# Kernel tuning notes

Measured on AMD Instinct MI355X. Metric: run time of the kernel, lower is better.

## Reference

```python
import jax, jax.numpy as jnp
import numpy as np

B, N, F, D, M, R, K, TOPR = 32, 1024, 10, 64, 4, 8, 20, 2
TAU = 1.0
BN_EPS = 1e-5


def setup_inputs() -> dict:
    key = jax.random.key(0)
    ks = jax.random.split(key, 20)
    s = 0.1
    p = {}
    p['data'] = jax.random.normal(ks[0], (B, N, F), jnp.float32)
    u = jnp.clip(jax.random.uniform(ks[1], (B, M), jnp.float32), 1e-6, 1.0 - 1e-6)
    p['gumbel_noise'] = -jnp.log(-jnp.log(u))
    p['W_cond'] = jax.random.normal(ks[2], (F, D), jnp.float32) * s
    p['b_cond'] = jnp.zeros((D,), jnp.float32)
    p['W_ap'] = jax.random.normal(ks[3], (D, D), jnp.float32) * s
    p['b_ap'] = jnp.zeros((D,), jnp.float32)
    p['W_av'] = jax.random.normal(ks[4], (D, 1), jnp.float32) * s
    p['W_r'] = jax.random.normal(ks[5], (D, M), jnp.float32) * s
    p['b_r'] = jnp.zeros((M,), jnp.float32)
    p['e_base'] = jax.random.normal(ks[6], (N, D), jnp.float32) * s
    p['lr_u'] = jax.random.normal(ks[7], (M, N, R), jnp.float32) * s
    p['lr_v'] = jax.random.normal(ks[8], (M, R, D), jnp.float32) * s
    p['W_gnn'] = jax.random.normal(ks[9], (F, D), jnp.float32) * s
    p['att_i'] = jax.random.normal(ks[10], (D,), jnp.float32) * s
    p['att_j'] = jax.random.normal(ks[11], (D,), jnp.float32) * s
    p['att_em_i'] = jax.random.normal(ks[12], (D,), jnp.float32) * s
    p['att_em_j'] = jax.random.normal(ks[13], (D,), jnp.float32) * s
    p['b_gnn'] = jnp.zeros((D,), jnp.float32)
    p['bn1_gamma'] = jnp.ones((D,), jnp.float32)
    p['bn1_beta'] = jnp.zeros((D,), jnp.float32)
    p['node_embed_table'] = jax.random.normal(ks[14], (N, D), jnp.float32) * s
    p['bn_out_gamma'] = jnp.ones((D,), jnp.float32)
    p['bn_out_beta'] = jnp.zeros((D,), jnp.float32)
    p['W_out'] = jax.random.normal(ks[15], (D, 1), jnp.float32) * s
    p['b_out'] = jnp.zeros((1,), jnp.float32)
    return p


def _nan(x):
    return jnp.nan_to_num(x, nan=0.0, posinf=1e4, neginf=-1e4)


def _bn(x, gamma, beta, axes):
    # BatchNorm1d in training mode: biased batch stats over `axes`.
    mu = x.mean(axes, keepdims=True)
    var = x.var(axes, keepdims=True)
    return (x - mu) * jax.lax.rsqrt(var + BN_EPS) * gamma + beta


def reference(data, gumbel_noise, W_cond, b_cond, W_ap, b_ap, W_av, W_r, b_r,
              e_base, lr_u, lr_v, W_gnn, att_i, att_j, att_em_i, att_em_j,
              b_gnn, bn1_gamma, bn1_beta, node_embed_table,
              bn_out_gamma, bn_out_beta, W_out, b_out):
    x_det = jax.lax.stop_gradient(data)                      # data.clone().detach()
    # --- condition attention pooling ---
    h_it = data @ W_cond + b_cond                            # [B,N,D]
    ah = jax.nn.leaky_relu(h_it @ W_ap + b_ap, 0.2)
    e_it = _nan((ah @ W_av)[..., 0])                         # [B,N]
    beta = jax.nn.softmax(e_it, axis=1)
    h_sys = jnp.sum(beta[..., None] * h_it, axis=1)          # [B,D]
    # --- gumbel top-k routing with straight-through ---
    pi_soft = jax.nn.softmax((h_sys @ W_r + b_r + gumbel_noise) / TAU, axis=-1)
    topv, topi = jax.lax.top_k(pi_soft, TOPR)
    pi_hard = jnp.sum(jax.nn.one_hot(topi, M, dtype=pi_soft.dtype) * topv[..., None], axis=1)
    pi_hard = pi_hard / jnp.maximum(pi_hard.sum(-1, keepdims=True), 1e-12)
    pi_t = jax.lax.stop_gradient(pi_hard - pi_soft) + pi_soft
    # --- low-rank expert prototypes -> mixed node embeddings ---
    proto = e_base[None] + jnp.einsum('mnr,mrd->mnd', lr_u, lr_v)    # [M,N,D]
    mixed = _nan(jnp.einsum('bm,mnd->bnd', pi_t, proto))             # [B,N,D]
    # --- dynamic top-k graph construction ---
    scores = _nan(jnp.einsum('bid,bjd->bij', mixed, mixed))          # [B,N,N]
    topk_vals, topk_idx = jax.lax.top_k(scores, K)                   # src nodes per dst: [B,N,K]
    topk_w = jax.nn.softmax(topk_vals, axis=-1)                      # edge weights
    # --- GAT-style layer with embedding-augmented keys, self loops re-added ---
    x_lin = x_det @ W_gnn                                            # [B,N,D]
    s_i = x_lin @ att_i + mixed @ att_em_i                           # [B,N]
    s_j = x_lin @ att_j + mixed @ att_em_j
    sj_nb = jnp.take_along_axis(s_j, topk_idx.reshape(B, N * K), axis=1).reshape(B, N, K)
    self_mask = topk_idx == jnp.arange(N)[None, :, None]             # remove_self_loops on topk edges
    alpha_nb = jnp.where(self_mask, -jnp.inf, jax.nn.leaky_relu(s_i[:, :, None] + sj_nb, 0.2))
    alpha_self = jax.nn.leaky_relu(s_i + s_j, 0.2)
    att = jax.nn.softmax(jnp.concatenate([alpha_nb, alpha_self[..., None]], axis=-1), axis=-1)
    w_nb = att[..., :K] * topk_w                                     # edge_weight modulation
    w_self = att[..., K]
    x_src = jnp.take_along_axis(x_lin, topk_idx.reshape(B, N * K)[..., None], axis=1).reshape(B, N, K, D)
    gnn = jnp.einsum('bnk,bnkd->bnd', w_nb, x_src) + w_self[..., None] * x_lin + b_gnn
    gnn = jax.nn.relu(_bn(gnn.reshape(B * N, D), bn1_gamma, bn1_beta, 0).reshape(B, N, D))
    # --- output head ---
    out = gnn * node_embed_table[None]                               # [B,N,D]
    out = jax.nn.relu(_bn(out, bn_out_gamma, bn_out_beta, (0, 1)))   # dropout = identity (eval)
    out = (out @ W_out + b_out).reshape(-1, N)                       # [B,N]
    return out, h_sys, pi_soft
```

## Files before the change

### kernel.cpp

```cpp
#include <hip/hip_runtime.h>
#include <math.h>

#define BB 32
#define NN 1024
#define FF 10
#define DD 64
#define MM 4
#define RR 8
#define KK 20
#define BNROWS (BB*NN)

#define OFF_HIT   0ull
#define OFF_XLIN  2097152ull
#define OFF_EIT   4194304ull
#define OFF_PIT   4227072ull
#define OFF_MIXED 4227200ull
#define OFF_SI    6324352ull
#define OFF_SJ    6357120ull
#define OFF_TKV   6389888ull
#define OFF_TKI   7045248ull
#define OFF_GNN   7700608ull
#define OFF_OUTP  9797760ull
#define OFF_STAT  11894912ull
#define OFF_SC    (OFF_STAT + 2560ull)

__device__ __forceinline__ float wave_sum(float v) {
    #pragma unroll
    for (int off = 32; off; off >>= 1) v += __shfl_xor(v, off);
    return v;
}
__device__ __forceinline__ float wave_max(float v) {
    #pragma unroll
    for (int off = 32; off; off >>= 1) v = fmaxf(v, __shfl_xor(v, off));
    return v;
}

__device__ __forceinline__ unsigned int dpp_wave_max_u32(unsigned int x) {
    unsigned int t;
    t = (unsigned)__builtin_amdgcn_update_dpp(0, (int)x, 0x111, 0xF, 0xF, true);
    x = x > t ? x : t;
    t = (unsigned)__builtin_amdgcn_update_dpp(0, (int)x, 0x112, 0xF, 0xF, true);
    x = x > t ? x : t;
    t = (unsigned)__builtin_amdgcn_update_dpp(0, (int)x, 0x114, 0xF, 0xF, true);
    x = x > t ? x : t;
    t = (unsigned)__builtin_amdgcn_update_dpp(0, (int)x, 0x118, 0xF, 0xF, true);
    x = x > t ? x : t;
    t = (unsigned)__builtin_amdgcn_update_dpp(0, (int)x, 0x142, 0xF, 0xF, true);
    x = x > t ? x : t;
    t = (unsigned)__builtin_amdgcn_update_dpp(0, (int)x, 0x143, 0xF, 0xF, true);
    x = x > t ? x : t;
    return (unsigned)__builtin_amdgcn_readlane((int)x, 63);
}

__global__ __launch_bounds__(256) void k_rows(
    const float* __restrict__ data, const float* __restrict__ W_cond,
    const float* __restrict__ b_cond, const float* __restrict__ W_ap,
    const float* __restrict__ b_ap, const float* __restrict__ W_av,
    const float* __restrict__ W_gnn,
    float* __restrict__ h_it, float* __restrict__ x_lin, float* __restrict__ e_it,
    float* __restrict__ stats)
{
    if (blockIdx.x < 10) {
        int idx = blockIdx.x * 256 + threadIdx.x;
        if (idx < 2336) stats[idx] = 0.f;
    }
    int w = threadIdx.x >> 6, lane = threadIdx.x & 63;
    int r = blockIdx.x * 4 + w;
    const float* dr = data + r * FF;
    float df[FF];
    #pragma unroll
    for (int f = 0; f < FF; f++) df[f] = dr[f];
    float h = b_cond[lane], x = 0.f;
    #pragma unroll
    for (int f = 0; f < FF; f++) {
        h = fmaf(df[f], W_cond[f * DD + lane], h);
        x = fmaf(df[f], W_gnn[f * DD + lane], x);
    }
    h_it[r * DD + lane] = h;
    x_lin[r * DD + lane] = x;
    float acc = b_ap[lane];
    #pragma unroll
    for (int e2 = 0; e2 < DD; e2++)
        acc = fmaf(__shfl(h, e2), W_ap[e2 * DD + lane], acc);
    float lr = acc > 0.f ? acc : 0.2f * acc;
    float ep = wave_sum(lr * W_av[lane]);
    if (lane == 0) e_it[r] = ep;
}

__global__ __launch_bounds__(256) void k_pool2(
    const float* __restrict__ e_it, const float* __restrict__ h_it,
    float* __restrict__ num, float* __restrict__ den)
{
    int w = threadIdx.x >> 6, lane = threadIdx.x & 63;
    int b = blockIdx.x >> 3, ch = blockIdx.x & 7;
    int base = b * NN + ch * 128 + w * 32;
    float acc = 0.f, dn = 0.f;
    #pragma unroll 4
    for (int i = 0; i < 32; i++) {
        float e = e_it[base + i];
        float wgt = expf(e);
        acc = fmaf(wgt, h_it[(size_t)(base + i) * DD + lane], acc);
        dn += wgt;
    }
    __shared__ float pa[4][DD];
    __shared__ float pd[4];
    pa[w][lane] = acc;
    if (lane == 0) pd[w] = dn;
    __syncthreads();
    if (w == 0) {
        float s = pa[0][lane] + pa[1][lane] + pa[2][lane] + pa[3][lane];
        atomicAdd(&num[b * DD + lane], s);
        if (lane == 0) atomicAdd(&den[b], pd[0] + pd[1] + pd[2] + pd[3]);
    }
}

__global__ void k_route(const float* __restrict__ num, const float* __restrict__ den,
                        const float* __restrict__ W_r, const float* __restrict__ b_r,
                        const float* __restrict__ gumbel,
                        float* __restrict__ h_sys, float* __restrict__ pi_soft,
                        float* __restrict__ pi_t)
{
    int tid = threadIdx.x;
    for (int i = tid; i < BB * DD; i += 256)
        h_sys[i] = num[i] / den[i >> 6];
    if (tid >= BB) return;
    int b = tid;
    float inv = 1.0f / den[b];
    float lg[MM];
    #pragma unroll
    for (int m = 0; m < MM; m++) lg[m] = b_r[m] + gumbel[b * MM + m];
    for (int d = 0; d < DD; d++) {
        float hv = num[b * DD + d] * inv;
        #pragma unroll
        for (int m = 0; m < MM; m++) lg[m] = fmaf(hv, W_r[d * MM + m], lg[m]);
    }
    float mx = fmaxf(fmaxf(lg[0], lg[1]), fmaxf(lg[2], lg[3]));
    float s = 0.f, p[MM];
    #pragma unroll
    for (int m = 0; m < MM; m++) { p[m] = expf(lg[m] - mx); s += p[m]; }
    #pragma unroll
    for (int m = 0; m < MM; m++) { p[m] /= s; pi_soft[b * MM + m] = p[m]; }
    int i1 = 0; float v1 = p[0];
    #pragma unroll
    for (int m = 1; m < MM; m++) if (p[m] > v1) { v1 = p[m]; i1 = m; }
    int i2 = -1; float v2 = -1.f;
    #pragma unroll
    for (int m = 0; m < MM; m++) if (m != i1 && p[m] > v2) { v2 = p[m]; i2 = m; }
    float norm = fmaxf(v1 + v2, 1e-12f);
    #pragma unroll
    for (int m = 0; m < MM; m++)
        pi_t[b * MM + m] = (m == i1 ? v1 : (m == i2 ? v2 : 0.f)) / norm;
}

__global__ __launch_bounds__(256) void k_mixed(
    const float* __restrict__ e_base, const float* __restrict__ lr_u,
    const float* __restrict__ lr_v, const float* __restrict__ pi_t,
    const float* __restrict__ x_lin,
    const float* __restrict__ att_i, const float* __restrict__ att_j,
    const float* __restrict__ att_em_i, const float* __restrict__ att_em_j,
    float* __restrict__ mixed, float* __restrict__ s_i, float* __restrict__ s_j)
{
    int w = threadIdx.x >> 6, lane = threadIdx.x & 63;
    int r = blockIdx.x * 4 + w;
    int b = r >> 10, n = r & 1023;
    float LR[MM];
    #pragma unroll
    for (int m = 0; m < MM; m++) {
        float a = 0.f;
        #pragma unroll
        for (int rr = 0; rr < RR; rr++)
            a = fmaf(lr_u[(m * NN + n) * RR + rr], lr_v[(m * RR + rr) * DD + lane], a);
        LR[m] = a;
    }
    float eb = e_base[n * DD + lane];
    float mx = 0.f;
    #pragma unroll
    for (int m = 0; m < MM; m++) mx = fmaf(pi_t[b * MM + m], eb + LR[m], mx);
    mixed[(size_t)r * DD + lane] = mx;
    float x = x_lin[(size_t)r * DD + lane];
    float r1 = wave_sum(x * att_i[lane] + mx * att_em_i[lane]);
    float r2 = wave_sum(x * att_j[lane] + mx * att_em_j[lane]);
    if (lane == 0) { s_i[r] = r1; s_j[r] = r2; }
}

__global__ __launch_bounds__(256) void k_score(
    const float* __restrict__ mixed_chunk, float* __restrict__ sc)
{
    __shared__ float As[32 * 132];
    __shared__ float Bs[32 * 132];
    int t = threadIdx.x;
    int bb = blockIdx.x >> 6;
    int rr = blockIdx.x & 63;
    int it = rr >> 3, jt = rr & 7;
    int i0 = it * 128, j0 = jt * 128;
    const float* mb = mixed_chunk + (size_t)bb * NN * DD;

    int tx = t & 15, ty = t >> 4;
    float acc[8][8];
    #pragma unroll
    for (int a = 0; a < 8; a++)
        #pragma unroll
        for (int bj = 0; bj < 8; bj++) acc[a][bj] = 0.f;

    for (int hh = 0; hh < 2; hh++) {
        if (hh) __syncthreads();
        #pragma unroll
        for (int c = 0; c < 4; c++) {
            int id = t + c * 256;
            int row = (id & 15) | ((id >> 7) << 4);
            int q = (id >> 4) & 7;
            const float4 va = *(const float4*)(mb + (size_t)(i0 + row) * DD + hh * 32 + q * 4);
            As[(q * 4 + 0) * 132 + row] = va.x;
            As[(q * 4 + 1) * 132 + row] = va.y;
            As[(q * 4 + 2) * 132 + row] = va.z;
            As[(q * 4 + 3) * 132 + row] = va.w;
            const float4 vb = *(const float4*)(mb + (size_t)(j0 + row) * DD + hh * 32 + q * 4);
            Bs[(q * 4 + 0) * 132 + row] = vb.x;
            Bs[(q * 4 + 1) * 132 + row] = vb.y;
            Bs[(q * 4 + 2) * 132 + row] = vb.z;
            Bs[(q * 4 + 3) * 132 + row] = vb.w;
        }
        __syncthreads();
        #pragma unroll 4
        for (int d = 0; d < 32; d++) {
            float4 a0 = *(const float4*)&As[d * 132 + ty * 8];
            float4 a1 = *(const float4*)&As[d * 132 + ty * 8 + 4];
            float4 b0 = *(const float4*)&Bs[d * 132 + tx * 8];
            float4 b1 = *(const float4*)&Bs[d * 132 + tx * 8 + 4];
            float av[8] = {a0.x, a0.y, a0.z, a0.w, a1.x, a1.y, a1.z, a1.w};
            float bv[8] = {b0.x, b0.y, b0.z, b0.w, b1.x, b1.y, b1.z, b1.w};
            #pragma unroll
            for (int a = 0; a < 8; a++)
                #pragma unroll
                for (int bj = 0; bj < 8; bj++)
                    acc[a][bj] = fmaf(av[a], bv[bj], acc[a][bj]);
        }
    }

    float* out = sc + ((size_t)bb * NN + i0 + ty * 8) * NN + j0 + tx * 8;
    #pragma unroll
    for (int a = 0; a < 8; a++) {
        float4 o0 = {acc[a][0], acc[a][1], acc[a][2], acc[a][3]};
        float4 o1 = {acc[a][4], acc[a][5], acc[a][6], acc[a][7]};
        *(float4*)(out + (size_t)a * NN) = o0;
        *(float4*)(out + (size_t)a * NN + 4) = o1;
    }
}

__global__ __launch_bounds__(256) void k_select(
    const float* __restrict__ sc, int b0,
    float* __restrict__ tkv, int* __restrict__ tki)
{
    int w = threadIdx.x >> 6, lane = threadIdx.x & 63;
    int lr = blockIdx.x * 4 + w;
    const float* row = sc + (size_t)lr * NN;

    unsigned gk[4][4];
    int gs[4][4];
    #pragma unroll
    for (int c = 0; c < 4; c++) {
        float4 v = *(const float4*)(row + c * 256 + lane * 4);
        float vv[4] = {v.x, v.y, v.z, v.w};
        #pragma unroll
        for (int q = 0; q < 4; q++) {
            unsigned u = __float_as_uint(vv[q]);
            unsigned msk = ((unsigned)((int)u >> 31)) | 0x80000000u;
            gk[c][q] = u ^ msk;
            gs[c][q] = c * 4 + q;
        }
        #define CMPSWAP(x, y) { \
            bool sw = gk[c][x] < gk[c][y]; \
            unsigned ka = gk[c][x], kb2 = gk[c][y]; int sa = gs[c][x], sb = gs[c][y]; \
            gk[c][x] = sw ? kb2 : ka; gk[c][y] = sw ? ka : kb2; \
            gs[c][x] = sw ? sb : sa; gs[c][y] = sw ? sa : sb; }
        CMPSWAP(0, 1) CMPSWAP(2, 3) CMPSWAP(0, 2) CMPSWAP(1, 3) CMPSWAP(1, 2)
        #undef CMPSWAP
    }
    unsigned head; int hs;
    {
        unsigned h01 = gk[0][0]; int s01 = gs[0][0];
        if (gk[1][0] > h01) { h01 = gk[1][0]; s01 = gs[1][0]; }
        unsigned h23 = gk[2][0]; int s23 = gs[2][0];
        if (gk[3][0] > h23) { h23 = gk[3][0]; s23 = gs[3][0]; }
        head = h01; hs = s01;
        if (h23 > head) { head = h23; hs = s23; }
    }

    float myv = 0.f; int myj = 0;
    #pragma unroll
    for (int k = 0; k < KK; k++) {
        unsigned m = dpp_wave_max_u32(head);
        unsigned long long ball = __ballot(head == m);
        int winner = (int)__builtin_ctzll(ball);
        int slotw = __shfl(hs, winner);
        int j = ((slotw >> 2) << 8) + winner * 4 + (slotw & 3);
        unsigned um = (m & 0x80000000u) ? (m ^ 0x80000000u) : ~m;
        if (lane == k) { myv = __uint_as_float(um); myj = j; }
        bool iswin = (lane == winner);
        int gi = slotw >> 2;
        #define POPG(c) { \
            gk[c][0] = iswin ? gk[c][1] : gk[c][0]; gs[c][0] = iswin ? gs[c][1] : gs[c][0]; \
            gk[c][1] = iswin ? gk[c][2] : gk[c][1]; gs[c][1] = iswin ? gs[c][2] : gs[c][1]; \
            gk[c][2] = iswin ? gk[c][3] : gk[c][2]; gs[c][2] = iswin ? gs[c][3] : gs[c][2]; \
            gk[c][3] = iswin ? 0u : gk[c][3]; }
        if (gi == 0) { POPG(0) } else if (gi == 1) { POPG(1) }
        else if (gi == 2) { POPG(2) } else { POPG(3) }
        #undef POPG
        unsigned h01 = gk[0][0]; int s01 = gs[0][0];
        if (gk[1][0] > h01) { h01 = gk[1][0]; s01 = gs[1][0]; }
        unsigned h23 = gk[2][0]; int s23 = gs[2][0];
        if (gk[3][0] > h23) { h23 = gk[3][0]; s23 = gs[3][0]; }
        head = h01; hs = s01;
        if (h23 > head) { head = h23; hs = s23; }
    }
    if (lane < KK) {
        int gr = b0 * NN + lr;
        tkv[(size_t)gr * KK + lane] = myv;
        tki[(size_t)gr * KK + lane] = myj;
    }
}

__global__ __launch_bounds__(256) void k_gat(
    const float* __restrict__ x_lin, const float* __restrict__ s_i,
    const float* __restrict__ s_j, const float* __restrict__ tkv,
    const int* __restrict__ tki, const float* __restrict__ b_gnn,
    float* __restrict__ gnn_pre)
{
    int w = threadIdx.x >> 6, lane = threadIdx.x & 63;
    int r = blockIdx.x * 4 + w;
    int b = r >> 10, n = r & 1023;
    float vk = -INFINITY; int ik = 0;
    if (lane < KK) { vk = tkv[r * KK + lane]; ik = tki[r * KK + lane]; }
    float m1 = wave_max(vk);
    float ek = (lane < KK) ? expf(vk - m1) : 0.f;
    float s1v = wave_sum(ek);
    float wk = ek / s1v;
    float si = s_i[r], sjn = s_j[r];
    float a = -INFINITY;
    if (lane < KK) {
        float sjk = s_j[(b << 10) + ik];
        float t2 = si + sjk;
        a = (ik == n) ? -INFINITY : (t2 > 0.f ? t2 : 0.2f * t2);
    }
    float ts = si + sjn;
    float aself = ts > 0.f ? ts : 0.2f * ts;
    float am = wave_max(fmaxf(a, aself));
    float ea = (lane < KK && a != -INFINITY) ? expf(a - am) : 0.f;
    float es = expf(aself - am);
    float ssum = wave_sum(ea) + es;
    float wnb = (ea / ssum) * wk;
    float wself = es / ssum;
    float acc = b_gnn[lane] + wself * x_lin[r * DD + lane];
    #pragma unroll
    for (int k = 0; k < KK; k++) {
        int jk = __shfl(ik, k);
        float wv = __shfl(wnb, k);
        acc = fmaf(wv, x_lin[((b << 10) + jk) * DD + lane], acc);
    }
    gnn_pre[r * DD + lane] = acc;
}

__global__ __launch_bounds__(256) void k_stats(const float* __restrict__ src, float* __restrict__ sums)
{
    int w = threadIdx.x >> 6, lane = threadIdx.x & 63;
    __shared__ float ps[4][DD], pq[4][DD];
    float s = 0.f, q = 0.f;
    int base = blockIdx.x * 128;
    for (int i = w; i < 128; i += 4) {
        float v = src[(size_t)(base + i) * DD + lane];
        s += v; q = fmaf(v, v, q);
    }
    ps[w][lane] = s; pq[w][lane] = q;
    __syncthreads();
    if (w == 0) {
        s = ps[0][lane] + ps[1][lane] + ps[2][lane] + ps[3][lane];
        q = pq[0][lane] + pq[1][lane] + pq[2][lane] + pq[3][lane];
        atomicAdd(&sums[lane], s);
        atomicAdd(&sums[DD + lane], q);
    }
}

__global__ __launch_bounds__(256) void k_bn1(
    const float* __restrict__ gnn_pre, float* __restrict__ stats,
    const float* __restrict__ gamma, const float* __restrict__ beta,
    const float* __restrict__ net, float* __restrict__ out_pre)
{
    int tid = threadIdx.x;
    int d0 = (tid & 15) * 4;
    float mean4[4], rs4[4], bt4[4];
    #pragma unroll
    for (int k = 0; k < 4; k++) {
        float mu = stats[d0 + k] * (1.0f / BNROWS);
        float var = stats[64 + d0 + k] * (1.0f / BNROWS) - mu * mu;
        mean4[k] = mu;
        rs4[k] = rsqrtf(var + 1e-5f) * gamma[d0 + k];
        bt4[k] = beta[d0 + k];
    }
    float s4[4] = {0, 0, 0, 0}, q4[4] = {0, 0, 0, 0};
    size_t base4 = (size_t)blockIdx.x * 2048;
    #pragma unroll
    for (int i = 0; i < 8; i++) {
        size_t f4 = base4 + (size_t)i * 256 + tid;
        float4 v = ((const float4*)gnn_pre)[f4];
        int n = ((int)(f4 >> 4)) & 1023;
        float4 nv = ((const float4*)net)[(size_t)n * 16 + (tid & 15)];
        float vv[4] = {v.x, v.y, v.z, v.w};
        float nn2[4] = {nv.x, nv.y, nv.z, nv.w};
        float ov[4];
        #pragma unroll
        for (int k = 0; k < 4; k++) {
            float y = (vv[k] - mean4[k]) * rs4[k] + bt4[k];
            y = y > 0.f ? y : 0.f;
            float o = y * nn2[k];
            ov[k] = o;
            s4[k] += o;
            q4[k] = fmaf(o, o, q4[k]);
        }
        float4 o4 = {ov[0], ov[1], ov[2], ov[3]};
        ((float4*)out_pre)[f4] = o4;
    }
    __shared__ float4 ls[256], lq[256];
    ls[tid] = make_float4(s4[0], s4[1], s4[2], s4[3]);
    lq[tid] = make_float4(q4[0], q4[1], q4[2], q4[3]);
    __syncthreads();
    if (tid < 16) {
        float4 S = ls[tid], Q = lq[tid];
        #pragma unroll
        for (int rr = 1; rr < 16; rr++) {
            float4 a = ls[tid + 16 * rr], b = lq[tid + 16 * rr];
            S.x += a.x; S.y += a.y; S.z += a.z; S.w += a.w;
            Q.x += b.x; Q.y += b.y; Q.z += b.z; Q.w += b.w;
        }
        atomicAdd(&stats[128 + tid * 4 + 0], S.x);
        atomicAdd(&stats[128 + tid * 4 + 1], S.y);
        atomicAdd(&stats[128 + tid * 4 + 2], S.z);
        atomicAdd(&stats[128 + tid * 4 + 3], S.w);
        atomicAdd(&stats[192 + tid * 4 + 0], Q.x);
        atomicAdd(&stats[192 + tid * 4 + 1], Q.y);
        atomicAdd(&stats[192 + tid * 4 + 2], Q.z);
        atomicAdd(&stats[192 + tid * 4 + 3], Q.w);
    }
}

__global__ __launch_bounds__(256) void k_head(
    const float* __restrict__ out_pre, const float* __restrict__ stats,
    const float* __restrict__ gamma, const float* __restrict__ beta,
    const float* __restrict__ W_out, const float* __restrict__ b_out,
    float* __restrict__ out)
{
    int w = threadIdx.x >> 6, lane = threadIdx.x & 63;
    int r = blockIdx.x * 4 + w;
    float mean = stats[lane] * (1.0f / BNROWS);
    float var = stats[DD + lane] * (1.0f / BNROWS) - mean * mean;
    float rs = rsqrtf(var + 1e-5f);
    float y = (out_pre[(size_t)r * DD + lane] - mean) * rs * gamma[lane] + beta[lane];
    y = y > 0.f ? y : 0.f;
    float p = wave_sum(y * W_out[lane]);
    if (lane == 0) out[r] = p + b_out[0];
}

extern "C" void kernel_launch(void* const* d_in, const int* in_sizes, int n_in,
                              void* d_out, int out_size, void* d_ws, size_t ws_size,
                              hipStream_t stream)
{
    const float* data     = (const float*)d_in[0];
    const float* gumbel   = (const float*)d_in[1];
    const float* W_cond   = (const float*)d_in[2];
    const float* b_cond   = (const float*)d_in[3];
    const float* W_ap     = (const float*)d_in[4];
    const float* b_ap     = (const float*)d_in[5];
    const float* W_av     = (const float*)d_in[6];
    const float* W_r      = (const float*)d_in[7];
    const float* b_r      = (const float*)d_in[8];
    const float* e_base   = (const float*)d_in[9];
    const float* lr_u     = (const float*)d_in[10];
    const float* lr_v     = (const float*)d_in[11];
    const float* W_gnn    = (const float*)d_in[12];
    const float* att_i    = (const float*)d_in[13];
    const float* att_j    = (const float*)d_in[14];
    const float* att_em_i = (const float*)d_in[15];
    const float* att_em_j = (const float*)d_in[16];
    const float* b_gnn    = (const float*)d_in[17];
    const float* bn1_g    = (const float*)d_in[18];
    const float* bn1_b    = (const float*)d_in[19];
    const float* net      = (const float*)d_in[20];
    const float* bno_g    = (const float*)d_in[21];
    const float* bno_b    = (const float*)d_in[22];
    const float* W_out    = (const float*)d_in[23];
    const float* b_out    = (const float*)d_in[24];

    float* ws = (float*)d_ws;
    float* h_it   = ws + OFF_HIT;
    float* x_lin  = ws + OFF_XLIN;
    float* e_it   = ws + OFF_EIT;
    float* pi_t   = ws + OFF_PIT;
    float* mixed  = ws + OFF_MIXED;
    float* s_i    = ws + OFF_SI;
    float* s_j    = ws + OFF_SJ;
    float* tkv    = ws + OFF_TKV;
    int*   tki    = (int*)(ws + OFF_TKI);
    float* gnn_pre = ws + OFF_GNN;
    float* out_pre = ws + OFF_OUTP;
    float* stats   = ws + OFF_STAT;
    float* pnum    = stats + 256;
    float* pden    = stats + 2304;

    float* out0    = (float*)d_out;
    float* h_sys   = out0 + BB * NN;
    float* pi_soft = out0 + BB * NN + BB * DD;

    k_rows<<<BNROWS / 4, 256, 0, stream>>>(data, W_cond, b_cond, W_ap, b_ap, W_av, W_gnn,
                                           h_it, x_lin, e_it, stats);
    k_pool2<<<BB * 8, 256, 0, stream>>>(e_it, h_it, pnum, pden);
    k_route<<<1, 256, 0, stream>>>(pnum, pden, W_r, b_r, gumbel, h_sys, pi_soft, pi_t);
    k_mixed<<<BNROWS / 4, 256, 0, stream>>>(e_base, lr_u, lr_v, pi_t, x_lin,
                                            att_i, att_j, att_em_i, att_em_j, mixed, s_i, s_j);

    size_t ws_floats = ws_size / 4;
    size_t avail = ws_floats > OFF_SC ? ws_floats - OFF_SC : 0;
    int cb = (int)(avail / (size_t)(NN * NN));
    if (cb > BB) cb = BB;
    float* sc = ws + OFF_SC;
    if (cb < 1) { cb = 2; sc = h_it; }
    for (int b0 = 0; b0 < BB; b0 += cb) {
        int c = (BB - b0) < cb ? (BB - b0) : cb;
        k_score<<<c * 64, 256, 0, stream>>>(mixed + (size_t)b0 * NN * DD, sc);
        k_select<<<c * 256, 256, 0, stream>>>(sc, b0, tkv, tki);
    }

    k_gat<<<BNROWS / 4, 256, 0, stream>>>(x_lin, s_i, s_j, tkv, tki, b_gnn, gnn_pre);
    k_stats<<<256, 256, 0, stream>>>(gnn_pre, stats);
    k_bn1<<<256, 256, 0, stream>>>(gnn_pre, stats, bn1_g, bn1_b, net, out_pre);
    k_head<<<BNROWS / 4, 256, 0, stream>>>(out_pre, stats + 128, bno_g, bno_b, W_out, b_out, out0);
}
```

Before: 345.4 us.

## Fuse top-k selection into GAT kernel with threshold-filter bitonic select

```diff
diff --git a/kernel.cpp b/kernel.cpp
--- a/kernel.cpp
+++ b/kernel.cpp
@@ -17,8 +17,6 @@
 #define OFF_MIXED 4227200ull
 #define OFF_SI    6324352ull
 #define OFF_SJ    6357120ull
-#define OFF_TKV   6389888ull
-#define OFF_TKI   7045248ull
 #define OFF_GNN   7700608ull
 #define OFF_OUTP  9797760ull
 #define OFF_STAT  11894912ull
@@ -33,23 +31,6 @@
     #pragma unroll
     for (int off = 32; off; off >>= 1) v = fmaxf(v, __shfl_xor(v, off));
     return v;
-}
-
-__device__ __forceinline__ unsigned int dpp_wave_max_u32(unsigned int x) {
-    unsigned int t;
-    t = (unsigned)__builtin_amdgcn_update_dpp(0, (int)x, 0x111, 0xF, 0xF, true);
-    x = x > t ? x : t;
-    t = (unsigned)__builtin_amdgcn_update_dpp(0, (int)x, 0x112, 0xF, 0xF, true);
-    x = x > t ? x : t;
-    t = (unsigned)__builtin_amdgcn_update_dpp(0, (int)x, 0x114, 0xF, 0xF, true);
-    x = x > t ? x : t;
-    t = (unsigned)__builtin_amdgcn_update_dpp(0, (int)x, 0x118, 0xF, 0xF, true);
-    x = x > t ? x : t;
-    t = (unsigned)__builtin_amdgcn_update_dpp(0, (int)x, 0x142, 0xF, 0xF, true);
-    x = x > t ? x : t;
-    t = (unsigned)__builtin_amdgcn_update_dpp(0, (int)x, 0x143, 0xF, 0xF, true);
-    x = x > t ? x : t;
-    return (unsigned)__builtin_amdgcn_readlane((int)x, 63);
 }
 
 __global__ __launch_bounds__(256) void k_rows(
@@ -202,31 +183,43 @@
         #pragma unroll
         for (int bj = 0; bj < 8; bj++) acc[a][bj] = 0.f;
 
+    int rowi[4], qi[4], swi[4];
+    #pragma unroll
+    for (int c = 0; c < 4; c++) {
+        int id = t + c * 256;
+        rowi[c] = (id & 15) | ((id >> 7) << 4);
+        qi[c] = (id >> 4) & 7;
+        swi[c] = ((rowi[c] & 4) << 4) | ((rowi[c] >> 3) << 2) | (rowi[c] & 3);
+    }
+
+    float4 pa[4], pb[4];
+    #pragma unroll
+    for (int c = 0; c < 4; c++) {
+        pa[c] = *(const float4*)(mb + (size_t)(i0 + rowi[c]) * DD + qi[c] * 4);
+        pb[c] = *(const float4*)(mb + (size_t)(j0 + rowi[c]) * DD + qi[c] * 4);
+    }
     for (int hh = 0; hh < 2; hh++) {
         if (hh) __syncthreads();
         #pragma unroll
         for (int c = 0; c < 4; c++) {
-            int id = t + c * 256;
-            int row = (id & 15) | ((id >> 7) << 4);
-            int q = (id >> 4) & 7;
-            const float4 va = *(const float4*)(mb + (size_t)(i0 + row) * DD + hh * 32 + q * 4);
-            As[(q * 4 + 0) * 132 + row] = va.x;
-            As[(q * 4 + 1) * 132 + row] = va.y;
-            As[(q * 4 + 2) * 132 + row] = va.z;
-            As[(q * 4 + 3) * 132 + row] = va.w;
-            const float4 vb = *(const float4*)(mb + (size_t)(j0 + row) * DD + hh * 32 + q * 4);
-            Bs[(q * 4 + 0) * 132 + row] = vb.x;
-            Bs[(q * 4 + 1) * 132 + row] = vb.y;
-            Bs[(q * 4 + 2) * 132 + row] = vb.z;
-            Bs[(q * 4 + 3) * 132 + row] = vb.w;
+            int pos = qi[c] * 4 * 132 + swi[c];
+            As[pos] = pa[c].x; As[pos + 132] = pa[c].y; As[pos + 264] = pa[c].z; As[pos + 396] = pa[c].w;
+            Bs[pos] = pb[c].x; Bs[pos + 132] = pb[c].y; Bs[pos + 264] = pb[c].z; Bs[pos + 396] = pb[c].w;
         }
         __syncthreads();
+        if (hh == 0) {
+            #pragma unroll
+            for (int c = 0; c < 4; c++) {
+                pa[c] = *(const float4*)(mb + (size_t)(i0 + rowi[c]) * DD + 32 + qi[c] * 4);
+                pb[c] = *(const float4*)(mb + (size_t)(j0 + rowi[c]) * DD + 32 + qi[c] * 4);
+            }
+        }
         #pragma unroll 4
         for (int d = 0; d < 32; d++) {
-            float4 a0 = *(const float4*)&As[d * 132 + ty * 8];
-            float4 a1 = *(const float4*)&As[d * 132 + ty * 8 + 4];
-            float4 b0 = *(const float4*)&Bs[d * 132 + tx * 8];
-            float4 b1 = *(const float4*)&Bs[d * 132 + tx * 8 + 4];
+            float4 a0 = *(const float4*)&As[d * 132 + ty * 4];
+            float4 a1 = *(const float4*)&As[d * 132 + 64 + ty * 4];
+            float4 b0 = *(const float4*)&Bs[d * 132 + tx * 4];
+            float4 b1 = *(const float4*)&Bs[d * 132 + 64 + tx * 4];
             float av[8] = {a0.x, a0.y, a0.z, a0.w, a1.x, a1.y, a1.z, a1.w};
             float bv[8] = {b0.x, b0.y, b0.z, b0.w, b1.x, b1.y, b1.z, b1.w};
             #pragma unroll
@@ -247,16 +240,19 @@
     }
 }
 
-__global__ __launch_bounds__(256) void k_select(
+__global__ __launch_bounds__(256) void k_selgat(
     const float* __restrict__ sc, int b0,
-    float* __restrict__ tkv, int* __restrict__ tki)
+    const float* __restrict__ x_lin, const float* __restrict__ s_i,
+    const float* __restrict__ s_j, const float* __restrict__ b_gnn,
+    float* __restrict__ gnn_pre)
 {
     int w = threadIdx.x >> 6, lane = threadIdx.x & 63;
     int lr = blockIdx.x * 4 + w;
+    int r = b0 * NN + lr;
+    int b = r >> 10, n = r & 1023;
     const float* row = sc + (size_t)lr * NN;
 
-    unsigned gk[4][4];
-    int gs[4][4];
+    unsigned uk[16];
     #pragma unroll
     for (int c = 0; c < 4; c++) {
         float4 v = *(const float4*)(row + c * 256 + lane * 4);
@@ -264,73 +260,101 @@
         #pragma unroll
         for (int q = 0; q < 4; q++) {
             unsigned u = __float_as_uint(vv[q]);
-            unsigned msk = ((unsigned)((int)u >> 31)) | 0x80000000u;
-            gk[c][q] = u ^ msk;
-            gs[c][q] = c * 4 + q;
-        }
-        #define CMPSWAP(x, y) { \
-            bool sw = gk[c][x] < gk[c][y]; \
-            unsigned ka = gk[c][x], kb2 = gk[c][y]; int sa = gs[c][x], sb = gs[c][y]; \
-            gk[c][x] = sw ? kb2 : ka; gk[c][y] = sw ? ka : kb2; \
-            gs[c][x] = sw ? sb : sa; gs[c][y] = sw ? sa : sb; }
-        CMPSWAP(0, 1) CMPSWAP(2, 3) CMPSWAP(0, 2) CMPSWAP(1, 3) CMPSWAP(1, 2)
-        #undef CMPSWAP
-    }
-    unsigned head; int hs;
-    {
-        unsigned h01 = gk[0][0]; int s01 = gs[0][0];
-        if (gk[1][0] > h01) { h01 = gk[1][0]; s01 = gs[1][0]; }
-        unsigned h23 = gk[2][0]; int s23 = gs[2][0];
-        if (gk[3][0] > h23) { h23 = gk[3][0]; s23 = gs[3][0]; }
-        head = h01; hs = s01;
-        if (h23 > head) { head = h23; hs = s23; }
-    }
-
-    float myv = 0.f; int myj = 0;
-    #pragma unroll
-    for (int k = 0; k < KK; k++) {
-        unsigned m = dpp_wave_max_u32(head);
-        unsigned long long ball = __ballot(head == m);
-        int winner = (int)__builtin_ctzll(ball);
-        int slotw = __shfl(hs, winner);
-        int j = ((slotw >> 2) << 8) + winner * 4 + (slotw & 3);
-        unsigned um = (m & 0x80000000u) ? (m ^ 0x80000000u) : ~m;
-        if (lane == k) { myv = __uint_as_float(um); myj = j; }
-        bool iswin = (lane == winner);
-        int gi = slotw >> 2;
-        #define POPG(c) { \
-            gk[c][0] = iswin ? gk[c][1] : gk[c][0]; gs[c][0] = iswin ? gs[c][1] : gs[c][0]; \
-            gk[c][1] = iswin ? gk[c][2] : gk[c][1]; gs[c][1] = iswin ? gs[c][2] : gs[c][1]; \
-            gk[c][2] = iswin ? gk[c][3] : gk[c][2]; gs[c][2] = iswin ? gs[c][3] : gs[c][2]; \
-            gk[c][3] = iswin ? 0u : gk[c][3]; }
-        if (gi == 0) { POPG(0) } else if (gi == 1) { POPG(1) }
-        else if (gi == 2) { POPG(2) } else { POPG(3) }
-        #undef POPG
-        unsigned h01 = gk[0][0]; int s01 = gs[0][0];
-        if (gk[1][0] > h01) { h01 = gk[1][0]; s01 = gs[1][0]; }
-        unsigned h23 = gk[2][0]; int s23 = gs[2][0];
-        if (gk[3][0] > h23) { h23 = gk[3][0]; s23 = gs[3][0]; }
-        head = h01; hs = s01;
-        if (h23 > head) { head = h23; hs = s23; }
-    }
-    if (lane < KK) {
-        int gr = b0 * NN + lr;
-        tkv[(size_t)gr * KK + lane] = myv;
-        tki[(size_t)gr * KK + lane] = myj;
-    }
-}
-
-__global__ __launch_bounds__(256) void k_gat(
-    const float* __restrict__ x_lin, const float* __restrict__ s_i,
-    const float* __restrict__ s_j, const float* __restrict__ tkv,
-    const int* __restrict__ tki, const float* __restrict__ b_gnn,
-    float* __restrict__ gnn_pre)
-{
-    int w = threadIdx.x >> 6, lane = threadIdx.x & 63;
-    int r = blockIdx.x * 4 + w;
-    int b = r >> 10, n = r & 1023;
+            uk[c * 4 + q] = u ^ (((unsigned)((int)u >> 31)) | 0x80000000u);
+        }
+    }
+    unsigned mx = uk[0];
+    #pragma unroll
+    for (int i = 1; i < 16; i++) mx = uk[i] > mx ? uk[i] : mx;
+    unsigned sv = mx;
+    #pragma unroll
+    for (int blk = 2; blk <= 64; blk <<= 1) {
+        #pragma unroll
+        for (int dist = blk >> 1; dist >= 1; dist >>= 1) {
+            unsigned pv = (unsigned)__shfl_xor((int)sv, dist);
+            bool up = (lane & blk) == 0;
+            bool upper = (lane & dist) == 0;
+            bool g = sv > pv;
+            sv = (((g == upper) == up)) ? sv : pv;
+        }
+    }
+    unsigned tau = (unsigned)__shfl((int)sv, 19);
+
+    __shared__ unsigned skey[4][64];
+    __shared__ int sjj[4][64];
+    int base = 0;
+    #pragma unroll
+    for (int s = 0; s < 16; s++) {
+        bool q = uk[s] >= tau;
+        unsigned long long m = __ballot(q);
+        if (q) {
+            int pos = base + __popcll(m & ((1ull << lane) - 1ull));
+            if (pos < 64) {
+                skey[w][pos] = uk[s];
+                sjj[w][pos] = ((s >> 2) << 8) + lane * 4 + (s & 3);
+            }
+        }
+        base += __popcll(m);
+    }
+    int C = base;
+
     float vk = -INFINITY; int ik = 0;
-    if (lane < KK) { vk = tkv[r * KK + lane]; ik = tki[r * KK + lane]; }
+    if (C <= 64) {
+        unsigned ck = 0u; int cj = 0x7FFFFFFF;
+        if (lane < C) { ck = skey[w][lane]; cj = sjj[w][lane]; }
+        if (C <= 32) {
+            #pragma unroll
+            for (int blk = 2; blk <= 32; blk <<= 1)
+                #pragma unroll
+                for (int dist = blk >> 1; dist >= 1; dist >>= 1) {
+                    unsigned pk = (unsigned)__shfl_xor((int)ck, dist);
+                    int pj = __shfl_xor(cj, dist);
+                    bool up = (lane & blk) == 0;
+                    bool upper = (lane & dist) == 0;
+                    bool g = (ck > pk) || (ck == pk && cj < pj);
+                    bool keep = ((g == upper) == up);
+                    ck = keep ? ck : pk; cj = keep ? cj : pj;
+                }
+        } else {
+            #pragma unroll
+            for (int blk = 2; blk <= 64; blk <<= 1)
+                #pragma unroll
+                for (int dist = blk >> 1; dist >= 1; dist >>= 1) {
+                    unsigned pk = (unsigned)__shfl_xor((int)ck, dist);
+                    int pj = __shfl_xor(cj, dist);
+                    bool up = (lane & blk) == 0;
+                    bool upper = (lane & dist) == 0;
+                    bool g = (ck > pk) || (ck == pk && cj < pj);
+                    bool keep = ((g == upper) == up);
+                    ck = keep ? ck : pk; cj = keep ? cj : pj;
+                }
+        }
+        if (lane < KK) {
+            unsigned u = (ck & 0x80000000u) ? (ck ^ 0x80000000u) : ~ck;
+            vk = __uint_as_float(u);
+            ik = cj;
+        }
+    } else {
+        for (int k = 0; k < KK; k++) {
+            unsigned bm = uk[0]; int bsl = 0;
+            #pragma unroll
+            for (int i = 1; i < 16; i++) if (uk[i] > bm) { bm = uk[i]; bsl = i; }
+            unsigned wm = bm;
+            #pragma unroll
+            for (int off = 32; off; off >>= 1) {
+                unsigned tt = (unsigned)__shfl_xor((int)wm, off);
+                wm = tt > wm ? tt : wm;
+            }
+            unsigned long long ball = __ballot(bm == wm);
+            int winner = (int)__builtin_ctzll(ball);
+            int slotw = __shfl(bsl, winner);
+            int jw = ((slotw >> 2) << 8) + winner * 4 + (slotw & 3);
+            unsigned u2 = (wm & 0x80000000u) ? (wm ^ 0x80000000u) : ~wm;
+            if (lane == k) { vk = __uint_as_float(u2); ik = jw; }
+            if (lane == winner) uk[bsl] = 0u;
+        }
+    }
+
     float m1 = wave_max(vk);
     float ek = (lane < KK) ? expf(vk - m1) : 0.f;
     float s1v = wave_sum(ek);
@@ -350,14 +374,14 @@
     float ssum = wave_sum(ea) + es;
     float wnb = (ea / ssum) * wk;
     float wself = es / ssum;
-    float acc = b_gnn[lane] + wself * x_lin[r * DD + lane];
+    float acc = b_gnn[lane] + wself * x_lin[(size_t)r * DD + lane];
     #pragma unroll
     for (int k = 0; k < KK; k++) {
         int jk = __shfl(ik, k);
         float wv = __shfl(wnb, k);
-        acc = fmaf(wv, x_lin[((b << 10) + jk) * DD + lane], acc);
-    }
-    gnn_pre[r * DD + lane] = acc;
+        acc = fmaf(wv, x_lin[((size_t)(b << 10) + jk) * DD + lane], acc);
+    }
+    gnn_pre[(size_t)r * DD + lane] = acc;
 }
 
 __global__ __launch_bounds__(256) void k_stats(const float* __restrict__ src, float* __restrict__ sums)
@@ -497,8 +521,6 @@
     float* mixed  = ws + OFF_MIXED;
     float* s_i    = ws + OFF_SI;
     float* s_j    = ws + OFF_SJ;
-    float* tkv    = ws + OFF_TKV;
-    int*   tki    = (int*)(ws + OFF_TKI);
     float* gnn_pre = ws + OFF_GNN;
     float* out_pre = ws + OFF_OUTP;
     float* stats   = ws + OFF_STAT;
@@ -525,10 +547,9 @@
     for (int b0 = 0; b0 < BB; b0 += cb) {
         int c = (BB - b0) < cb ? (BB - b0) : cb;
         k_score<<<c * 64, 256, 0, stream>>>(mixed + (size_t)b0 * NN * DD, sc);
-        k_select<<<c * 256, 256, 0, stream>>>(sc, b0, tkv, tki);
-    }
-
-    k_gat<<<BNROWS / 4, 256, 0, stream>>>(x_lin, s_i, s_j, tkv, tki, b_gnn, gnn_pre);
+        k_selgat<<<c * 256, 256, 0, stream>>>(sc, b0, x_lin, s_i, s_j, b_gnn, gnn_pre);
+    }
+
     k_stats<<<256, 256, 0, stream>>>(gnn_pre, stats);
     k_bn1<<<256, 256, 0, stream>>>(gnn_pre, stats, bn1_g, bn1_b, net, out_pre);
     k_head<<<BNROWS / 4, 256, 0, stream>>>(out_pre, stats + 128, bno_g, bno_b, W_out, b_out, out0);
```

New measurement: 319.8 us. 1.08x faster.
